# Kernel optimization log

Measured on AMD Instinct MI355X. Metric: run time of the kernel, lower is better.

The kernel has to match this reference:

```python
import jax, jax.numpy as jnp
import numpy as np

N, E, D = 10000, 160000, 512


def setup_inputs() -> dict:
    key = jax.random.key(0)
    ks = jax.random.split(key, 5)
    x = jax.random.normal(ks[0], (N, D), dtype=jnp.float32)
    edge_index = jax.random.randint(ks[1], (2, E), 0, N, dtype=jnp.int32)
    W = jax.random.normal(ks[2], (D, D), dtype=jnp.float32) * (1.0 / np.sqrt(D))
    a_src = jax.random.normal(ks[3], (D,), dtype=jnp.float32) * 0.1
    a_dst = jax.random.normal(ks[4], (D,), dtype=jnp.float32) * 0.1
    bias = jnp.zeros((D,), dtype=jnp.float32)
    return {"x": x, "edge_index": edge_index, "W": W,
            "a_src": a_src, "a_dst": a_dst, "bias": bias}


def reference(x, edge_index, W, a_src, a_dst, bias):
    n = x.shape[0]
    # PyG GATConv default: add self-loops
    loops = jnp.arange(n, dtype=edge_index.dtype)
    src = jnp.concatenate([edge_index[0], loops])  # [E+N]
    dst = jnp.concatenate([edge_index[1], loops])  # [E+N]

    h = x @ W.T                                    # [N, D] linear projection
    e_src = h @ a_src                              # [N]
    e_dst = h @ a_dst                              # [N]
    e = e_src[src] + e_dst[dst]                    # [E+N]
    neg_slope = 0.2
    e = jnp.where(e > 0, e, neg_slope * e)         # leaky_relu

    # per-destination softmax (stable); self-loops guarantee non-empty segments
    m = jax.ops.segment_max(e, dst, num_segments=n)
    e = jnp.exp(e - m[dst])
    s = jax.ops.segment_sum(e, dst, num_segments=n)
    alpha = e / s[dst]                             # [E+N]

    msg = alpha[:, None] * h[src]                  # [E+N, D]
    out = jax.ops.segment_sum(msg, dst, num_segments=n) + bias  # [N, D]

    # module forward: x + elu(gat(x, edge_index))
    return x + jax.nn.elu(out)
```

## Files before the change

### kernel.cpp

```cpp
#include <hip/hip_runtime.h>
#include <hip/hip_bf16.h>

using bf16x8 = __attribute__((ext_vector_type(8))) __bf16;
using f32x4  = __attribute__((ext_vector_type(4))) float;
typedef unsigned int u32;

#define DFEAT 512
#define SLOTS 64

static __device__ __forceinline__ unsigned short f2bfbits(float f) {
    union { float f; unsigned int u; } v; v.f = f;
    unsigned int u = v.u;
    unsigned int r = (u + 0x7fffu + ((u >> 16) & 1u)) >> 16;
    return (unsigned short)r;
}

static __device__ __forceinline__ bf16x8 cvt8(float4 u, float4 v) {
    bf16x8 r;
    r[0] = (__bf16)u.x; r[1] = (__bf16)u.y; r[2] = (__bf16)u.z; r[3] = (__bf16)u.w;
    r[4] = (__bf16)v.x; r[5] = (__bf16)v.y; r[6] = (__bf16)v.z; r[7] = (__bf16)v.w;
    return r;
}

static __device__ __forceinline__ void gload16(const unsigned short* g, unsigned short* l) {
    __builtin_amdgcn_global_load_lds(
        (const __attribute__((address_space(1))) u32*)g,
        (__attribute__((address_space(3))) u32*)l, 16, 0, 0);
}

__global__ __launch_bounds__(256) void prep_kernel(
    const float* __restrict__ w, unsigned short* __restrict__ Wb,
    const int* __restrict__ srcv, const int* __restrict__ dstv,
    int* __restrict__ cur, int* __restrict__ slot,
    int nw4, int E, int T)
{
    int i = blockIdx.x * 256 + threadIdx.x;
    if (i < nw4) {
        float4 v = ((const float4*)w)[i];
        ushort4 u;
        u.x = f2bfbits(v.x); u.y = f2bfbits(v.y);
        u.z = f2bfbits(v.z); u.w = f2bfbits(v.w);
        ((ushort4*)Wb)[i] = u;
    }
    if (i < T) {
        int s, d;
        if (i < E) { s = srcv[i]; d = dstv[i]; }
        else       { s = d = i - E; }
        int pos = atomicAdd(&cur[d], 1);
        if (pos < SLOTS) slot[(size_t)d * SLOTS + pos] = s;
    }
}

__global__ __launch_bounds__(256, 3) void gemm_h_kernel(
    const float* __restrict__ Xf, const unsigned short* __restrict__ Wm,
    const float* __restrict__ avs, const float* __restrict__ avd,
    unsigned short* __restrict__ H, float* __restrict__ es, float* __restrict__ ed,
    int N)
{
    __shared__ __align__(16) unsigned short Asm[2][128 * 64];
    __shared__ __align__(16) unsigned short Bsm[2][64 * 64];

    int L = blockIdx.x;
    int xcd = L & 7;
    int q   = L >> 3;
    int rpan = (q >> 3) * 8 + xcd;
    int cpan = q & 7;
    int rowPanels = (N + 127) >> 7;
    if (rpan >= rowPanels) return;
    int bm = rpan * 128;
    int bn = cpan * 64;

    int tid  = threadIdx.x;
    int wave = tid >> 6;
    int lane = tid & 63;
    int l15  = lane & 15;
    int quad = lane >> 4;

    int srow   = lane >> 3;
    int schunk = (lane & 7) ^ srow;
    const unsigned short* gB0 = Wm + (size_t)(bn + wave * 16 + srow) * DFEAT + schunk * 8;
    const unsigned short* gB1 = gB0 + (size_t)8 * DFEAT;

    auto stageB = [&](int buf, int s) {
        int ko = s * 64;
        gload16(gB0 + ko, &Bsm[buf][(wave * 16 + 0) * 64]);
        gload16(gB1 + ko, &Bsm[buf][(wave * 16 + 8) * 64]);
    };

    int arl   = lane >> 1;
    int ac0   = (lane & 1) * 4;
    int arow  = bm + wave * 32 + arl;
    arow = arow < N ? arow : N - 1;
    const float* gA = Xf + (size_t)arow * DFEAT + ac0 * 8;
    int ldsrow = wave * 32 + arl;
    char* AbW0 = (char*)&Asm[0][0] + ldsrow * 128;
    char* AbW1 = (char*)&Asm[1][0] + ldsrow * 128;
    int axor = arl & 7;

    float4 av[8];
    auto aload = [&](int s) {
        const float* p = gA + s * 64;
        #pragma unroll
        for (int i = 0; i < 4; ++i) {
            av[2 * i]     = *(const float4*)(p + i * 8);
            av[2 * i + 1] = *(const float4*)(p + i * 8 + 4);
        }
    };
    auto awrite = [&](int buf) {
        char* Ab = buf ? AbW1 : AbW0;
        #pragma unroll
        for (int i = 0; i < 4; ++i) {
            bf16x8 o = cvt8(av[2 * i], av[2 * i + 1]);
            *(bf16x8*)(Ab + (((ac0 + i) ^ axor) * 16)) = o;
        }
    };

    f32x4 acc[2][4] = {};
    int xa = l15 & 7;
    int aoff0 = (wave * 32 +  0 + l15) * 128;
    int aoff1 = (wave * 32 + 16 + l15) * 128;

    auto compute = [&](int buf) {
        const char* Ab = (const char*)&Asm[buf][0];
        const char* Bb = (const char*)&Bsm[buf][0];
        #pragma unroll
        for (int ks = 0; ks < 2; ++ks) {
            int cb = ((ks * 4 + quad) ^ xa) * 16;
            bf16x8 a0 = *(const bf16x8*)(Ab + aoff0 + cb);
            bf16x8 a1 = *(const bf16x8*)(Ab + aoff1 + cb);
            bf16x8 b0 = *(const bf16x8*)(Bb + (0 * 16 + l15) * 128 + cb);
            bf16x8 b1 = *(const bf16x8*)(Bb + (1 * 16 + l15) * 128 + cb);
            bf16x8 b2 = *(const bf16x8*)(Bb + (2 * 16 + l15) * 128 + cb);
            bf16x8 b3 = *(const bf16x8*)(Bb + (3 * 16 + l15) * 128 + cb);
            acc[0][0] = __builtin_amdgcn_mfma_f32_16x16x32_bf16(a0, b0, acc[0][0], 0, 0, 0);
            acc[1][0] = __builtin_amdgcn_mfma_f32_16x16x32_bf16(a1, b0, acc[1][0], 0, 0, 0);
            acc[0][1] = __builtin_amdgcn_mfma_f32_16x16x32_bf16(a0, b1, acc[0][1], 0, 0, 0);
            acc[1][1] = __builtin_amdgcn_mfma_f32_16x16x32_bf16(a1, b1, acc[1][1], 0, 0, 0);
            acc[0][2] = __builtin_amdgcn_mfma_f32_16x16x32_bf16(a0, b2, acc[0][2], 0, 0, 0);
            acc[1][2] = __builtin_amdgcn_mfma_f32_16x16x32_bf16(a1, b2, acc[1][2], 0, 0, 0);
            acc[0][3] = __builtin_amdgcn_mfma_f32_16x16x32_bf16(a0, b3, acc[0][3], 0, 0, 0);
            acc[1][3] = __builtin_amdgcn_mfma_f32_16x16x32_bf16(a1, b3, acc[1][3], 0, 0, 0);
        }
    };

    stageB(0, 0);
    aload(0);
    awrite(0);
    __syncthreads();
    int buf = 0;
    for (int s = 0; s < 7; ++s) {
        stageB(buf ^ 1, s + 1);
        aload(s + 1);
        compute(buf);
        awrite(buf ^ 1);
        __syncthreads();
        buf ^= 1;
    }
    compute(buf);

    float as[4], ad[4];
    #pragma unroll
    for (int nt = 0; nt < 4; ++nt) {
        as[nt] = avs[bn + nt * 16 + l15];
        ad[nt] = avd[bn + nt * 16 + l15];
    }

    #pragma unroll
    for (int mt = 0; mt < 2; ++mt) {
        int rbase = bm + wave * 32 + mt * 16 + quad * 4;
        #pragma unroll
        for (int nt = 0; nt < 4; ++nt) {
            int col = bn + nt * 16 + l15;
            #pragma unroll
            for (int r = 0; r < 4; ++r) {
                int row = rbase + r;
                if (row < N) H[(size_t)row * DFEAT + col] = f2bfbits(acc[mt][nt][r]);
            }
        }
        #pragma unroll
        for (int r = 0; r < 4; ++r) {
            float ps = acc[mt][0][r] * as[0] + acc[mt][1][r] * as[1]
                     + acc[mt][2][r] * as[2] + acc[mt][3][r] * as[3];
            float pd = acc[mt][0][r] * ad[0] + acc[mt][1][r] * ad[1]
                     + acc[mt][2][r] * ad[2] + acc[mt][3][r] * ad[3];
            #pragma unroll
            for (int m = 1; m < 16; m <<= 1) {
                ps += __shfl_xor(ps, m);
                pd += __shfl_xor(pd, m);
            }
            int row = rbase + r;
            if (l15 == 0 && row < N) {
                atomicAdd(&es[row], ps);
                atomicAdd(&ed[row], pd);
            }
        }
    }
}

__global__ __launch_bounds__(256) void aggregate_kernel(
    const unsigned short* __restrict__ H, const float* __restrict__ x,
    const float* __restrict__ bias,
    const int* __restrict__ cur, const int* __restrict__ slot,
    const float* __restrict__ es, const float* __restrict__ ed,
    float* __restrict__ out, int N)
{
    int node = (blockIdx.x * 256 + threadIdx.x) >> 6;
    int lane = threadIdx.x & 63;
    if (node >= N) return;

    int k = cur[node];
    if (k > SLOTS) k = SLOTS;

    int   s = 0;
    float w = 0.f;
    if (lane < k) {
        s = slot[(size_t)node * SLOTS + lane];
        float e = es[s] + ed[node];
        e = e > 0.f ? e : 0.2f * e;
        w = __expf(e);
    }
    float denom = w;
    #pragma unroll
    for (int off = 32; off > 0; off >>= 1) denom += __shfl_xor(denom, off);
    float inv = 1.0f / denom;

    float a[8] = {};
    const unsigned short* Hl = H + lane * 8;

    auto fma8 = [&](uint4 hv, float wj) {
        a[0] += wj * __uint_as_float(hv.x << 16);
        a[1] += wj * __uint_as_float(hv.x & 0xffff0000u);
        a[2] += wj * __uint_as_float(hv.y << 16);
        a[3] += wj * __uint_as_float(hv.y & 0xffff0000u);
        a[4] += wj * __uint_as_float(hv.z << 16);
        a[5] += wj * __uint_as_float(hv.z & 0xffff0000u);
        a[6] += wj * __uint_as_float(hv.w << 16);
        a[7] += wj * __uint_as_float(hv.w & 0xffff0000u);
    };

    int j = 0;
    for (; j + 7 < k; j += 8) {
        int   s0 = __shfl(s, j),     s1 = __shfl(s, j + 1);
        int   s2 = __shfl(s, j + 2), s3 = __shfl(s, j + 3);
        int   s4 = __shfl(s, j + 4), s5 = __shfl(s, j + 5);
        int   s6 = __shfl(s, j + 6), s7 = __shfl(s, j + 7);
        float w0 = __shfl(w, j),     w1 = __shfl(w, j + 1);
        float w2 = __shfl(w, j + 2), w3 = __shfl(w, j + 3);
        float w4 = __shfl(w, j + 4), w5 = __shfl(w, j + 5);
        float w6 = __shfl(w, j + 6), w7 = __shfl(w, j + 7);
        uint4 h0 = *(const uint4*)(Hl + (size_t)s0 * DFEAT);
        uint4 h1 = *(const uint4*)(Hl + (size_t)s1 * DFEAT);
        uint4 h2 = *(const uint4*)(Hl + (size_t)s2 * DFEAT);
        uint4 h3 = *(const uint4*)(Hl + (size_t)s3 * DFEAT);
        uint4 h4 = *(const uint4*)(Hl + (size_t)s4 * DFEAT);
        uint4 h5 = *(const uint4*)(Hl + (size_t)s5 * DFEAT);
        uint4 h6 = *(const uint4*)(Hl + (size_t)s6 * DFEAT);
        uint4 h7 = *(const uint4*)(Hl + (size_t)s7 * DFEAT);
        fma8(h0, w0); fma8(h1, w1); fma8(h2, w2); fma8(h3, w3);
        fma8(h4, w4); fma8(h5, w5); fma8(h6, w6); fma8(h7, w7);
    }
    if (j + 3 < k) {
        int   s0 = __shfl(s, j),     s1 = __shfl(s, j + 1);
        int   s2 = __shfl(s, j + 2), s3 = __shfl(s, j + 3);
        float w0 = __shfl(w, j),     w1 = __shfl(w, j + 1);
        float w2 = __shfl(w, j + 2), w3 = __shfl(w, j + 3);
        uint4 h0 = *(const uint4*)(Hl + (size_t)s0 * DFEAT);
        uint4 h1 = *(const uint4*)(Hl + (size_t)s1 * DFEAT);
        uint4 h2 = *(const uint4*)(Hl + (size_t)s2 * DFEAT);
        uint4 h3 = *(const uint4*)(Hl + (size_t)s3 * DFEAT);
        fma8(h0, w0); fma8(h1, w1); fma8(h2, w2); fma8(h3, w3);
        j += 4;
    }
    for (; j < k; ++j) {
        uint4 hv = *(const uint4*)(Hl + (size_t)__shfl(s, j) * DFEAT);
        fma8(hv, __shfl(w, j));
    }

    int c = lane * 8;
    float4 b0 = *(const float4*)(bias + c);
    float4 b1 = *(const float4*)(bias + c + 4);
    float4 x0 = *(const float4*)(x + (size_t)node * DFEAT + c);
    float4 x1 = *(const float4*)(x + (size_t)node * DFEAT + c + 4);
    float r[8];
    r[0] = a[0] * inv + b0.x; r[1] = a[1] * inv + b0.y;
    r[2] = a[2] * inv + b0.z; r[3] = a[3] * inv + b0.w;
    r[4] = a[4] * inv + b1.x; r[5] = a[5] * inv + b1.y;
    r[6] = a[6] * inv + b1.z; r[7] = a[7] * inv + b1.w;
    #pragma unroll
    for (int i = 0; i < 8; ++i)
        r[i] = r[i] > 0.f ? r[i] : __expf(r[i]) - 1.f;
    float4 o0 = make_float4(x0.x + r[0], x0.y + r[1], x0.z + r[2], x0.w + r[3]);
    float4 o1 = make_float4(x1.x + r[4], x1.y + r[5], x1.z + r[6], x1.w + r[7]);
    *(float4*)(out + (size_t)node * DFEAT + c)     = o0;
    *(float4*)(out + (size_t)node * DFEAT + c + 4) = o1;
}

extern "C" void kernel_launch(void* const* d_in, const int* in_sizes, int n_in,
                              void* d_out, int out_size, void* d_ws, size_t ws_size,
                              hipStream_t stream)
{
    const float* x    = (const float*)d_in[0];
    const int*   edge = (const int*)d_in[1];
    const float* Wm   = (const float*)d_in[2];
    const float* avs  = (const float*)d_in[3];
    const float* avd  = (const float*)d_in[4];
    const float* bias = (const float*)d_in[5];

    const int D = DFEAT;
    const int N = in_sizes[0] / D;
    const int E = in_sizes[1] / 2;
    const int T = E + N;
    const int* srcv = edge;
    const int* dstv = edge + E;

    char* ws = (char*)d_ws;
    size_t off = 0;
    auto alloc = [&](size_t bytes) -> char* {
        char* p = ws + off;
        off += (bytes + 255) & ~(size_t)255;
        return p;
    };
    int*   cur  = (int*)alloc((size_t)N * 3 * 4);
    float* es   = (float*)(cur + N);
    float* ed   = es + N;
    int*   slot = (int*)alloc((size_t)N * SLOTS * 4);
    unsigned short* Wb = (unsigned short*)alloc((size_t)D * D * 2);
    unsigned short* H  = (unsigned short*)alloc((size_t)N * D * 2);

    hipMemsetAsync(cur, 0, (size_t)N * 3 * 4, stream);

    int nw4   = (D * D) / 4;
    int grid0 = (nw4 > T ? nw4 : T);
    prep_kernel<<<dim3((grid0 + 255) / 256), 256, 0, stream>>>(
        Wm, Wb, srcv, dstv, cur, slot, nw4, E, T);

    int rowPanels  = (N + 127) / 128;
    int rowPanels8 = ((rowPanels + 7) / 8) * 8;
    gemm_h_kernel<<<dim3(rowPanels8 * 8), 256, 0, stream>>>(
        x, Wb, avs, avd, H, es, ed, N);
    aggregate_kernel<<<dim3((N * 64 + 255) / 256), 256, 0, stream>>>(
        H, x, bias, cur, slot, es, ed, (float*)d_out, N);
}
```

Before: 148.0 us.

## Stage fp32 A tiles directly to LDS and convert to bf16 at compute

```diff
diff --git a/kernel.cpp b/kernel.cpp
--- a/kernel.cpp
+++ b/kernel.cpp
@@ -23,6 +23,11 @@
 }
 
 static __device__ __forceinline__ void gload16(const unsigned short* g, unsigned short* l) {
+    __builtin_amdgcn_global_load_lds(
+        (const __attribute__((address_space(1))) u32*)g,
+        (__attribute__((address_space(3))) u32*)l, 16, 0, 0);
+}
+static __device__ __forceinline__ void gload16f(const float* g, float* l) {
     __builtin_amdgcn_global_load_lds(
         (const __attribute__((address_space(1))) u32*)g,
         (__attribute__((address_space(3))) u32*)l, 16, 0, 0);
@@ -51,14 +56,14 @@
     }
 }
 
-__global__ __launch_bounds__(256, 3) void gemm_h_kernel(
+__global__ __launch_bounds__(256, 4) void gemm_h_kernel(
     const float* __restrict__ Xf, const unsigned short* __restrict__ Wm,
     const float* __restrict__ avs, const float* __restrict__ avd,
     unsigned short* __restrict__ H, float* __restrict__ es, float* __restrict__ ed,
     int N)
 {
-    __shared__ __align__(16) unsigned short Asm[2][128 * 64];
-    __shared__ __align__(16) unsigned short Bsm[2][64 * 64];
+    __shared__ __align__(16) float          As[2][128 * 32];
+    __shared__ __align__(16) unsigned short Bs[2][64 * 32];
 
     int L = blockIdx.x;
     int xcd = L & 7;
@@ -76,83 +81,73 @@
     int l15  = lane & 15;
     int quad = lane >> 4;
 
-    int srow   = lane >> 3;
-    int schunk = (lane & 7) ^ srow;
-    const unsigned short* gB0 = Wm + (size_t)(bn + wave * 16 + srow) * DFEAT + schunk * 8;
-    const unsigned short* gB1 = gB0 + (size_t)8 * DFEAT;
-
-    auto stageB = [&](int buf, int s) {
-        int ko = s * 64;
-        gload16(gB0 + ko, &Bsm[buf][(wave * 16 + 0) * 64]);
-        gload16(gB1 + ko, &Bsm[buf][(wave * 16 + 8) * 64]);
-    };
-
-    int arl   = lane >> 1;
-    int ac0   = (lane & 1) * 4;
-    int arow  = bm + wave * 32 + arl;
-    arow = arow < N ? arow : N - 1;
-    const float* gA = Xf + (size_t)arow * DFEAT + ac0 * 8;
-    int ldsrow = wave * 32 + arl;
-    char* AbW0 = (char*)&Asm[0][0] + ldsrow * 128;
-    char* AbW1 = (char*)&Asm[1][0] + ldsrow * 128;
-    int axor = arl & 7;
-
-    float4 av[8];
-    auto aload = [&](int s) {
-        const float* p = gA + s * 64;
-        #pragma unroll
-        for (int i = 0; i < 4; ++i) {
-            av[2 * i]     = *(const float4*)(p + i * 8);
-            av[2 * i + 1] = *(const float4*)(p + i * 8 + 4);
-        }
-    };
-    auto awrite = [&](int buf) {
-        char* Ab = buf ? AbW1 : AbW0;
-        #pragma unroll
-        for (int i = 0; i < 4; ++i) {
-            bf16x8 o = cvt8(av[2 * i], av[2 * i + 1]);
-            *(bf16x8*)(Ab + (((ac0 + i) ^ axor) * 16)) = o;
-        }
+    int arow8  = lane >> 3;
+    int achunk = (lane & 7) ^ arow8;
+    const float* gA0;
+    const float* gA1;
+    const float* gA2;
+    const float* gA3;
+    {
+        int r0 = bm + wave * 32 +  0 + arow8; r0 = r0 < N ? r0 : N - 1;
+        int r1 = bm + wave * 32 +  8 + arow8; r1 = r1 < N ? r1 : N - 1;
+        int r2 = bm + wave * 32 + 16 + arow8; r2 = r2 < N ? r2 : N - 1;
+        int r3 = bm + wave * 32 + 24 + arow8; r3 = r3 < N ? r3 : N - 1;
+        gA0 = Xf + (size_t)r0 * DFEAT + achunk * 4;
+        gA1 = Xf + (size_t)r1 * DFEAT + achunk * 4;
+        gA2 = Xf + (size_t)r2 * DFEAT + achunk * 4;
+        gA3 = Xf + (size_t)r3 * DFEAT + achunk * 4;
+    }
+    int brow4  = lane >> 2;
+    int bchunk = (lane & 3) ^ (brow4 & 3);
+    const unsigned short* gB = Wm + (size_t)(bn + wave * 16 + brow4) * DFEAT + bchunk * 8;
+
+    auto stage = [&](int buf, int s) {
+        int koA = s * 32;
+        gload16f(gA0 + koA, &As[buf][(wave * 32 +  0) * 32]);
+        gload16f(gA1 + koA, &As[buf][(wave * 32 +  8) * 32]);
+        gload16f(gA2 + koA, &As[buf][(wave * 32 + 16) * 32]);
+        gload16f(gA3 + koA, &As[buf][(wave * 32 + 24) * 32]);
+        gload16(gB + s * 32, &Bs[buf][(wave * 16) * 32]);
     };
 
     f32x4 acc[2][4] = {};
     int xa = l15 & 7;
+    int xb = l15 & 3;
     int aoff0 = (wave * 32 +  0 + l15) * 128;
     int aoff1 = (wave * 32 + 16 + l15) * 128;
 
     auto compute = [&](int buf) {
-        const char* Ab = (const char*)&Asm[buf][0];
-        const char* Bb = (const char*)&Bsm[buf][0];
-        #pragma unroll
-        for (int ks = 0; ks < 2; ++ks) {
-            int cb = ((ks * 4 + quad) ^ xa) * 16;
-            bf16x8 a0 = *(const bf16x8*)(Ab + aoff0 + cb);
-            bf16x8 a1 = *(const bf16x8*)(Ab + aoff1 + cb);
-            bf16x8 b0 = *(const bf16x8*)(Bb + (0 * 16 + l15) * 128 + cb);
-            bf16x8 b1 = *(const bf16x8*)(Bb + (1 * 16 + l15) * 128 + cb);
-            bf16x8 b2 = *(const bf16x8*)(Bb + (2 * 16 + l15) * 128 + cb);
-            bf16x8 b3 = *(const bf16x8*)(Bb + (3 * 16 + l15) * 128 + cb);
-            acc[0][0] = __builtin_amdgcn_mfma_f32_16x16x32_bf16(a0, b0, acc[0][0], 0, 0, 0);
-            acc[1][0] = __builtin_amdgcn_mfma_f32_16x16x32_bf16(a1, b0, acc[1][0], 0, 0, 0);
-            acc[0][1] = __builtin_amdgcn_mfma_f32_16x16x32_bf16(a0, b1, acc[0][1], 0, 0, 0);
-            acc[1][1] = __builtin_amdgcn_mfma_f32_16x16x32_bf16(a1, b1, acc[1][1], 0, 0, 0);
-            acc[0][2] = __builtin_amdgcn_mfma_f32_16x16x32_bf16(a0, b2, acc[0][2], 0, 0, 0);
-            acc[1][2] = __builtin_amdgcn_mfma_f32_16x16x32_bf16(a1, b2, acc[1][2], 0, 0, 0);
-            acc[0][3] = __builtin_amdgcn_mfma_f32_16x16x32_bf16(a0, b3, acc[0][3], 0, 0, 0);
-            acc[1][3] = __builtin_amdgcn_mfma_f32_16x16x32_bf16(a1, b3, acc[1][3], 0, 0, 0);
-        }
+        const char* Ab = (const char*)&As[buf][0];
+        const char* Bb = (const char*)&Bs[buf][0];
+        int ca0 = ((2 * quad)     ^ xa) * 16;
+        int ca1 = ((2 * quad + 1) ^ xa) * 16;
+        float4 a0lo = *(const float4*)(Ab + aoff0 + ca0);
+        float4 a0hi = *(const float4*)(Ab + aoff0 + ca1);
+        float4 a1lo = *(const float4*)(Ab + aoff1 + ca0);
+        float4 a1hi = *(const float4*)(Ab + aoff1 + ca1);
+        int cb = (quad ^ xb) * 16;
+        bf16x8 b0 = *(const bf16x8*)(Bb + (0 * 16 + l15) * 64 + cb);
+        bf16x8 b1 = *(const bf16x8*)(Bb + (1 * 16 + l15) * 64 + cb);
+        bf16x8 b2 = *(const bf16x8*)(Bb + (2 * 16 + l15) * 64 + cb);
+        bf16x8 b3 = *(const bf16x8*)(Bb + (3 * 16 + l15) * 64 + cb);
+        bf16x8 a0 = cvt8(a0lo, a0hi);
+        bf16x8 a1 = cvt8(a1lo, a1hi);
+        acc[0][0] = __builtin_amdgcn_mfma_f32_16x16x32_bf16(a0, b0, acc[0][0], 0, 0, 0);
+        acc[1][0] = __builtin_amdgcn_mfma_f32_16x16x32_bf16(a1, b0, acc[1][0], 0, 0, 0);
+        acc[0][1] = __builtin_amdgcn_mfma_f32_16x16x32_bf16(a0, b1, acc[0][1], 0, 0, 0);
+        acc[1][1] = __builtin_amdgcn_mfma_f32_16x16x32_bf16(a1, b1, acc[1][1], 0, 0, 0);
+        acc[0][2] = __builtin_amdgcn_mfma_f32_16x16x32_bf16(a0, b2, acc[0][2], 0, 0, 0);
+        acc[1][2] = __builtin_amdgcn_mfma_f32_16x16x32_bf16(a1, b2, acc[1][2], 0, 0, 0);
+        acc[0][3] = __builtin_amdgcn_mfma_f32_16x16x32_bf16(a0, b3, acc[0][3], 0, 0, 0);
+        acc[1][3] = __builtin_amdgcn_mfma_f32_16x16x32_bf16(a1, b3, acc[1][3], 0, 0, 0);
     };
 
-    stageB(0, 0);
-    aload(0);
-    awrite(0);
+    stage(0, 0);
     __syncthreads();
     int buf = 0;
-    for (int s = 0; s < 7; ++s) {
-        stageB(buf ^ 1, s + 1);
-        aload(s + 1);
+    for (int s = 0; s < 15; ++s) {
+        stage(buf ^ 1, s + 1);
         compute(buf);
-        awrite(buf ^ 1);
         __syncthreads();
         buf ^= 1;
     }
```

Measured after the change: 133.5 us. -9.8%, faster.
